# Kernel optimization log

Measured on AMD Instinct MI355X. Metric: run time of the kernel, lower is better.

## Reference

```python
import jax, jax.numpy as jnp
import numpy as np


def setup_inputs() -> dict:
    key = jax.random.key(0)
    k1, k2 = jax.random.split(key)
    x = jax.random.normal(k1, (64, 1024, 2), dtype=jnp.float32)
    target = jax.random.normal(k2, (64, 1024, 2), dtype=jnp.float32)
    return {"x": x, "target": target}


def reference(x, target):
    # x, target: [B, N, 2] snake control points (uniform nb_cp = N).
    B, N, _ = x.shape
    target = target.astype(x.dtype)
    # Pairwise L2 distances between every pred point and every ref point.
    # D[b, j, k] = ||x[b, j] - target[b, k]||  -> [B, N, N]
    D = jnp.linalg.norm(x[:, :, None, :] - target[:, None, :, :], axis=-1)
    # Cyclic shift s maps ref_s[j] = target[(j - s) mod N] (torch.roll shifts=1, s times).
    j = jnp.arange(N)
    idx = (j[None, :] - j[:, None]) % N  # [S, N], idx[s, j] = (j - s) % N
    # shift_means[b, s] = (1/N) * sum_j D[b, j, (j - s) % N]
    shift_means = D[:, j[None, :], idx].sum(axis=-1) / N  # [B, N]
    min_loss = jnp.min(shift_means, axis=-1)  # [B]
    return jnp.mean(min_loss)
```

## Files before the change

kernel.cpp:

```cpp
#include <hip/hip_runtime.h>
#include <math.h>


#define BATCH 64
#define NPT   1024
#define SGRP  4
#define JGRP  4
#define TPB   256
#define JLEN  (NPT / JGRP)
#define WIN   512

__global__ __launch_bounds__(TPB) void snake_partial(
    const float2* __restrict__ x, const float2* __restrict__ tgt,
    float* __restrict__ partial) {
  const int b   = blockIdx.x;
  const int sg  = blockIdx.y;
  const int jg  = blockIdx.z;
  const int tid = threadIdx.x;
  const int j0  = jg * JLEN;
  const int s0  = sg * TPB;

  __shared__ float4 t4[WIN];

  const float2* tb = tgt + b * NPT;
  const int kb = (j0 - s0 - 255) & (NPT - 1);
  for (int w = tid; w < WIN; w += TPB) {
    const float2 a = tb[(kb + w) & (NPT - 1)];
    const float2 c = tb[(kb + w + 1) & (NPT - 1)];
    t4[w] = make_float4(a.x, a.y, c.x, c.y);
  }
  __syncthreads();

  const float4* xg = (const float4*)(x + b * NPT + j0);

  float acc0 = 0.f, acc1 = 0.f;
  const int off0 = 255 - tid;
#pragma unroll 8
  for (int jl = 0; jl < JLEN; jl += 2) {
    const float4 tp = t4[off0 + jl];
    const float4 xp = xg[jl >> 1];
    const float dx0 = xp.x - tp.x, dy0 = xp.y - tp.y;
    const float dx1 = xp.z - tp.z, dy1 = xp.w - tp.w;
    acc0 += __builtin_amdgcn_sqrtf(fmaf(dx0, dx0, dy0 * dy0));
    acc1 += __builtin_amdgcn_sqrtf(fmaf(dx1, dx1, dy1 * dy1));
  }
  partial[(b * JGRP + jg) * NPT + s0 + tid] = acc0 + acc1;
}

__global__ __launch_bounds__(TPB) void snake_min(
    const float* __restrict__ partial, float* __restrict__ bmin) {
  const int b   = blockIdx.x;
  const int tid = threadIdx.x;
  float m = 3.4e38f;
  for (int si = 0; si < NPT / TPB; ++si) {
    const int s = si * TPB + tid;
    float tot = 0.f;
#pragma unroll
    for (int jg = 0; jg < JGRP; ++jg)
      tot += partial[(b * JGRP + jg) * NPT + s];
    m = fminf(m, tot);
  }
  for (int o = 32; o > 0; o >>= 1)
    m = fminf(m, __shfl_down(m, o));
  __shared__ float red[4];
  if ((tid & 63) == 0) red[tid >> 6] = m;
  __syncthreads();
  if (tid == 0)
    bmin[b] = fminf(fminf(red[0], red[1]), fminf(red[2], red[3]));
}

__global__ void snake_final(const float* __restrict__ bmin,
                            float* __restrict__ out) {
  float v = bmin[threadIdx.x];
  for (int o = 32; o > 0; o >>= 1)
    v += __shfl_down(v, o);
  if (threadIdx.x == 0)
    out[0] = v * (1.0f / ((float)NPT * (float)BATCH));
}

extern "C" void kernel_launch(void* const* d_in, const int* in_sizes, int n_in,
                              void* d_out, int out_size, void* d_ws, size_t ws_size,
                              hipStream_t stream) {
  const float2* x   = (const float2*)d_in[0];
  const float2* tgt = (const float2*)d_in[1];
  float* partial = (float*)d_ws;
  float* bmin    = partial + BATCH * JGRP * NPT;
  float* out     = (float*)d_out;

  dim3 g1(BATCH, SGRP, JGRP);
  snake_partial<<<g1, TPB, 0, stream>>>(x, tgt, partial);
  snake_min<<<BATCH, TPB, 0, stream>>>(partial, bmin);
  snake_final<<<1, 64, 0, stream>>>(bmin, out);
}
```

Baseline: 72.33 us.

## Reuse each target LDS load across four shift groups per thread

Each thread now handles four shifts 256 apart, so one shared-memory target read serves four x rows that are read through separate pointers. The j dimension is split into 16 groups instead of 4 and the separate shift-group grid dimension is removed. The partial buffer layout becomes jg-major, and the min reduction is split across four blocks per batch whose results are combined in the final kernel. The aim is to cut LDS traffic and staging overhead per unit of work, at the cost of more global x loads and a larger partial buffer for the reduction to read.

```diff
diff --git a/kernel.cpp b/kernel.cpp
--- a/kernel.cpp
+++ b/kernel.cpp
@@ -4,77 +4,89 @@
 
 #define BATCH 64
 #define NPT   1024
-#define SGRP  4
-#define JGRP  4
 #define TPB   256
+#define G     4
+#define JGRP  16
 #define JLEN  (NPT / JGRP)
-#define WIN   512
+#define TWIN  (JLEN + 256)
 
 __global__ __launch_bounds__(TPB) void snake_partial(
     const float2* __restrict__ x, const float2* __restrict__ tgt,
     float* __restrict__ partial) {
   const int b   = blockIdx.x;
-  const int sg  = blockIdx.y;
-  const int jg  = blockIdx.z;
+  const int jg  = blockIdx.y;
   const int tid = threadIdx.x;
   const int j0  = jg * JLEN;
-  const int s0  = sg * TPB;
 
-  __shared__ float4 t4[WIN];
-
+  __shared__ float4 t4[TWIN];
   const float2* tb = tgt + b * NPT;
-  const int kb = (j0 - s0 - 255) & (NPT - 1);
-  for (int w = tid; w < WIN; w += TPB) {
+  const int kb = (j0 - 255) & (NPT - 1);
+  for (int w = tid; w < TWIN; w += TPB) {
     const float2 a = tb[(kb + w) & (NPT - 1)];
     const float2 c = tb[(kb + w + 1) & (NPT - 1)];
     t4[w] = make_float4(a.x, a.y, c.x, c.y);
   }
   __syncthreads();
 
-  const float4* xg = (const float4*)(x + b * NPT + j0);
+  const float4* xg[G];
+#pragma unroll
+  for (int g = 0; g < G; ++g) {
+    const int cg = (j0 + 256 * g) & (NPT - 1);
+    xg[g] = (const float4*)(x + b * NPT + cg);
+  }
 
-  float acc0 = 0.f, acc1 = 0.f;
+  float2 acc[G];
+#pragma unroll
+  for (int g = 0; g < G; ++g) acc[g] = make_float2(0.f, 0.f);
+
   const int off0 = 255 - tid;
-#pragma unroll 8
+#pragma unroll 4
   for (int jl = 0; jl < JLEN; jl += 2) {
     const float4 tp = t4[off0 + jl];
-    const float4 xp = xg[jl >> 1];
-    const float dx0 = xp.x - tp.x, dy0 = xp.y - tp.y;
-    const float dx1 = xp.z - tp.z, dy1 = xp.w - tp.w;
-    acc0 += __builtin_amdgcn_sqrtf(fmaf(dx0, dx0, dy0 * dy0));
-    acc1 += __builtin_amdgcn_sqrtf(fmaf(dx1, dx1, dy1 * dy1));
+#pragma unroll
+    for (int g = 0; g < G; ++g) {
+      const float4 xp = xg[g][jl >> 1];
+      const float dx0 = xp.x - tp.x, dy0 = xp.y - tp.y;
+      const float dx1 = xp.z - tp.z, dy1 = xp.w - tp.w;
+      acc[g].x += __builtin_amdgcn_sqrtf(fmaf(dx0, dx0, dy0 * dy0));
+      acc[g].y += __builtin_amdgcn_sqrtf(fmaf(dx1, dx1, dy1 * dy1));
+    }
   }
-  partial[(b * JGRP + jg) * NPT + s0 + tid] = acc0 + acc1;
+
+  float* prow = partial + (jg * BATCH + b) * NPT;
+#pragma unroll
+  for (int g = 0; g < G; ++g)
+    prow[tid + 256 * g] = acc[g].x + acc[g].y;
 }
 
 __global__ __launch_bounds__(TPB) void snake_min(
-    const float* __restrict__ partial, float* __restrict__ bmin) {
+    const float* __restrict__ partial, float* __restrict__ bmin2) {
   const int b   = blockIdx.x;
+  const int sg  = blockIdx.y;
   const int tid = threadIdx.x;
-  float m = 3.4e38f;
-  for (int si = 0; si < NPT / TPB; ++si) {
-    const int s = si * TPB + tid;
-    float tot = 0.f;
+  const int s   = sg * TPB + tid;
+  float tot = 0.f;
 #pragma unroll
-    for (int jg = 0; jg < JGRP; ++jg)
-      tot += partial[(b * JGRP + jg) * NPT + s];
-    m = fminf(m, tot);
-  }
+  for (int jg = 0; jg < JGRP; ++jg)
+    tot += partial[(jg * BATCH + b) * NPT + s];
+  float m = tot;
   for (int o = 32; o > 0; o >>= 1)
     m = fminf(m, __shfl_down(m, o));
   __shared__ float red[4];
   if ((tid & 63) == 0) red[tid >> 6] = m;
   __syncthreads();
   if (tid == 0)
-    bmin[b] = fminf(fminf(red[0], red[1]), fminf(red[2], red[3]));
+    bmin2[b * 4 + sg] = fminf(fminf(red[0], red[1]), fminf(red[2], red[3]));
 }
 
-__global__ void snake_final(const float* __restrict__ bmin,
+__global__ void snake_final(const float* __restrict__ bmin2,
                             float* __restrict__ out) {
-  float v = bmin[threadIdx.x];
+  const int b = threadIdx.x;
+  float v = fminf(fminf(bmin2[b * 4 + 0], bmin2[b * 4 + 1]),
+                  fminf(bmin2[b * 4 + 2], bmin2[b * 4 + 3]));
   for (int o = 32; o > 0; o >>= 1)
     v += __shfl_down(v, o);
-  if (threadIdx.x == 0)
+  if (b == 0)
     out[0] = v * (1.0f / ((float)NPT * (float)BATCH));
 }
 
@@ -84,11 +96,12 @@
   const float2* x   = (const float2*)d_in[0];
   const float2* tgt = (const float2*)d_in[1];
   float* partial = (float*)d_ws;
-  float* bmin    = partial + BATCH * JGRP * NPT;
+  float* bmin2   = partial + JGRP * BATCH * NPT;
   float* out     = (float*)d_out;
 
-  dim3 g1(BATCH, SGRP, JGRP);
+  dim3 g1(BATCH, JGRP);
   snake_partial<<<g1, TPB, 0, stream>>>(x, tgt, partial);
-  snake_min<<<BATCH, TPB, 0, stream>>>(partial, bmin);
-  snake_final<<<1, 64, 0, stream>>>(bmin, out);
+  dim3 g2(BATCH, 4);
+  snake_min<<<g2, TPB, 0, stream>>>(partial, bmin2);
+  snake_final<<<1, 64, 0, stream>>>(bmin2, out);
 }
```

Result: no change. 71.43 us (-1.2%).
